# Kernel optimization log

Measured on AMD Instinct MI355X. Metric: run time of the kernel, lower is better.

## Reference

```python
import jax, jax.numpy as jnp
import numpy as np

H = 12  # num_heads

def setup_inputs() -> dict:
    key = jax.random.key(0)
    ks = jax.random.split(key, 6)
    B, L, D = 2, 2048, 768
    x = jax.random.normal(ks[0], (B, L, D), dtype=jnp.float32)
    token_sizes = jax.random.uniform(ks[1], (B, L), dtype=jnp.float32)
    attn_mask = jnp.triu(jnp.ones((L, L), dtype=bool), k=1)
    key_padding_mask = jnp.zeros((B, L), dtype=bool)
    qkv_w = jax.random.normal(ks[2], (3 * D, D), dtype=jnp.float32) * (D ** -0.5)
    qkv_b = jax.random.normal(ks[3], (3 * D,), dtype=jnp.float32) * 0.02
    proj_w = jax.random.normal(ks[4], (D, D), dtype=jnp.float32) * (D ** -0.5)
    proj_b = jax.random.normal(ks[5], (D,), dtype=jnp.float32) * 0.02
    return {"x": x, "token_sizes": token_sizes, "attn_mask": attn_mask,
            "key_padding_mask": key_padding_mask, "qkv_w": qkv_w, "qkv_b": qkv_b,
            "proj_w": proj_w, "proj_b": proj_b}

def reference(x, token_sizes, attn_mask, key_padding_mask, qkv_w, qkv_b, proj_w, proj_b):
    B, L, D = x.shape
    hd = D // H
    scale = hd ** -0.5
    qkv = (x @ qkv_w.T + qkv_b).reshape(B, L, 3, H, hd)
    qkv = jnp.transpose(qkv, (2, 0, 3, 1, 4))  # [3, B, H, L, hd]
    q, k, v = qkv[0], qkv[1], qkv[2]
    logits = jnp.einsum('bhqd,bhkd->bhqk', q, k) * scale  # [B,H,L,L]
    neg = jnp.finfo(logits.dtype).min
    logits = jnp.where(attn_mask[None, None, :, :], neg, logits)
    logits = jnp.where(key_padding_mask[:, None, None, :], neg, logits)
    logits = logits + jnp.log(jnp.clip(token_sizes, 1e-8))[:, None, None, :]
    attn = jax.nn.softmax(logits, axis=-1)
    out = jnp.einsum('bhqk,bhkd->bhqd', attn, v)
    out = jnp.transpose(out, (0, 2, 1, 3)).reshape(B, L, D)
    out = out @ proj_w.T + proj_b
    k_merge = k.mean(axis=1)  # [B, L, hd]
    return (out, k_merge)
```

## Files before the change

kernel.cpp:

```cpp
#include <hip/hip_runtime.h>
#include <hip/hip_bf16.h>

typedef unsigned short u16;
typedef __bf16 bf16x8 __attribute__((ext_vector_type(8)));
typedef float f32x4 __attribute__((ext_vector_type(4)));

#define QSCALE (0.125f * 1.44269504088896340736f)

__device__ __forceinline__ u16 f2bf(float f) {
    __hip_bfloat16 h = __float2bfloat16(f);
    return __builtin_bit_cast(u16, h);
}
__device__ __forceinline__ float bf2f(u16 u) {
    unsigned int x = ((unsigned int)u) << 16;
    return __builtin_bit_cast(float, x);
}
__device__ __forceinline__ bf16x8 ld_bf8(const u16* p) {
    uint4 u = *reinterpret_cast<const uint4*>(p);
    return __builtin_bit_cast(bf16x8, u);
}
__device__ __forceinline__ bf16x8 pack8f(f32x4 a, f32x4 b) {
    union { bf16x8 v; u16 u[8]; } r;
    #pragma unroll
    for (int i = 0; i < 4; i++) { r.u[i] = f2bf(a[i]); r.u[4+i] = f2bf(b[i]); }
    return r.v;
}
__device__ __forceinline__ bf16x8 pack8u(ushort4 a, ushort4 b) {
    union { bf16x8 v; ushort4 u[2]; } r;
    r.u[0] = a; r.u[1] = b;
    return r.v;
}

#define GLOAD_LDS16(g, l) __builtin_amdgcn_global_load_lds( \
    (const __attribute__((address_space(1))) unsigned int*)(g), \
    (__attribute__((address_space(3))) unsigned int*)(l), 16, 0, 0)

template<int N> __device__ __forceinline__ void s_wait_vmcnt() {
    if constexpr (N == 0)      asm volatile("s_waitcnt vmcnt(0)" ::: "memory");
    else if constexpr (N == 3) asm volatile("s_waitcnt vmcnt(3)" ::: "memory");
    else if constexpr (N == 4) asm volatile("s_waitcnt vmcnt(4)" ::: "memory");
    else                       asm volatile("s_waitcnt vmcnt(8)" ::: "memory");
}
__device__ __forceinline__ void s_bar() {
    __builtin_amdgcn_sched_barrier(0);
    __builtin_amdgcn_s_barrier();
    __builtin_amdgcn_sched_barrier(0);
}
__device__ __forceinline__ void s_wait_lgkm0_bar() {
    asm volatile("s_waitcnt lgkmcnt(0)" ::: "memory");
    __builtin_amdgcn_sched_barrier(0);
    __builtin_amdgcn_s_barrier();
    __builtin_amdgcn_sched_barrier(0);
}

__global__ __launch_bounds__(256) void prep_kernel(
    const float* __restrict__ x, const float* __restrict__ qkvw,
    const float* __restrict__ projw, const float* __restrict__ ts,
    const unsigned char* __restrict__ kpm,
    u16* __restrict__ Xb, u16* __restrict__ Wq, u16* __restrict__ Wp,
    float* __restrict__ tsw, u16* __restrict__ tbf, int* __restrict__ qcount)
{
    int i = blockIdx.x * 256 + threadIdx.x;
    if (i == 0) *qcount = 0;
    const int XC4 = 4096 * 768 / 4;
    const int WQ4 = 2304 * 768 / 4;
    const int WP4 = 768 * 768 / 4;
    const float* src = nullptr; u16* dst = nullptr;
    if (i < XC4) { src = x; dst = Xb; }
    else {
        i -= XC4;
        if (i < WQ4) { src = qkvw; dst = Wq; }
        else {
            i -= WQ4;
            if (i < WP4) { src = projw; dst = Wp; }
            else {
                i -= WP4;
                if (i < 1024) {
                    float4 t = *(const float4*)(ts + i*4);
                    uchar4 k = *(const uchar4*)(kpm + i*4);
                    float4 r;
                    r.x = k.x ? 0.f : fmaxf(t.x, 1e-8f);
                    r.y = k.y ? 0.f : fmaxf(t.y, 1e-8f);
                    r.z = k.z ? 0.f : fmaxf(t.z, 1e-8f);
                    r.w = k.w ? 0.f : fmaxf(t.w, 1e-8f);
                    *(float4*)(tsw + i*4) = r;
                    ushort4 o;
                    o.x = f2bf(r.x); o.y = f2bf(r.y);
                    o.z = f2bf(r.z); o.w = f2bf(r.w);
                    *(ushort4*)(tbf + i*4) = o;
                }
                return;
            }
        }
    }
    float4 v = *(const float4*)(src + i*4);
    ushort4 o;
    o.x = f2bf(v.x); o.y = f2bf(v.y); o.z = f2bf(v.z); o.w = f2bf(v.w);
    *(ushort4*)(dst + i*4) = o;
}

template<int EPI, int MI>
__global__ __launch_bounds__(256, 2) void gemm_bt(
    const u16* __restrict__ A, const u16* __restrict__ Bm,
    const float* __restrict__ bias, const float* __restrict__ tsw,
    u16* __restrict__ Qb, u16* __restrict__ Kb, u16* __restrict__ Vt,
    float* __restrict__ outp)
{
    constexpr int BM = MI * 32;
    constexpr int ACALLS = MI / 2;
    constexpr int SA = ACALLS + 2;
    constexpr int NT = 24;
    __shared__ u16 As[2][BM * 32];
    __shared__ u16 Bs[2][128 * 32];
    const int K = 768;
    const int tid = threadIdx.x;
    const int nwg = gridDim.x * gridDim.y;
    const int flat = blockIdx.y * gridDim.x + blockIdx.x;
    const int per = nwg >> 3;
    const int swz = (flat & 7) * per + (flat >> 3);
    const int m0 = (swz / gridDim.x) * BM;
    const int n0 = (swz % gridDim.x) * 128;
    const int w = tid >> 6, lane = tid & 63;
    const int wr = (w >> 1) * (MI * 16), wc = (w & 1) * 64;
    const int g = lane >> 4, l16 = lane & 15;

    const int srow = lane >> 2;
    const int scol = (lane & 3) * 8;
    const u16* gA[ACALLS];
    #pragma unroll
    for (int c = 0; c < ACALLS; c++)
        gA[c] = A + (size_t)(m0 + (c*4 + w)*16 + srow) * K + scol;
    const u16* gB[2];
    #pragma unroll
    for (int c = 0; c < 2; c++)
        gB[c] = Bm + (size_t)(n0 + (c*4 + w)*16 + srow) * K + scol;

#define GSTAGE(buf, kk) do { \
    _Pragma("unroll") \
    for (int c = 0; c < ACALLS; c++) \
        GLOAD_LDS16(gA[c] + (kk), &As[buf][(c*4 + w) * 512]); \
    _Pragma("unroll") \
    for (int c = 0; c < 2; c++) \
        GLOAD_LDS16(gB[c] + (kk), &Bs[buf][(c*4 + w) * 512]); } while (0)

    f32x4 acc[MI][4] = {};
    GSTAGE(0, 0);
    GSTAGE(1, 32);
    for (int it = 0; it < NT; it++) {
        const int k0 = it * 32;
        const int cur = it & 1;
        if (it < NT - 1) s_wait_vmcnt<SA>();
        else             s_wait_vmcnt<0>();
        s_bar();
        bf16x8 af[MI], bfr[4];
        #pragma unroll
        for (int i = 0; i < MI; i++) af[i]  = ld_bf8(&As[cur][(wr + i*16 + l16)*32 + g*8]);
        #pragma unroll
        for (int j = 0; j < 4; j++)  bfr[j] = ld_bf8(&Bs[cur][(wc + j*16 + l16)*32 + g*8]);
        s_wait_lgkm0_bar();
        if (it + 2 < NT) GSTAGE(cur, k0 + 64);
        __builtin_amdgcn_s_setprio(1);
        #pragma unroll
        for (int i = 0; i < MI; i++)
            #pragma unroll
            for (int j = 0; j < 4; j++)
                acc[i][j] = __builtin_amdgcn_mfma_f32_16x16x32_bf16(af[i], bfr[j], acc[i][j], 0, 0, 0);
        __builtin_amdgcn_s_setprio(0);
    }
#undef GSTAGE

    #pragma unroll
    for (int j = 0; j < 4; j++) {
        const int n = n0 + wc + j*16 + l16;
        const float bs = bias[n];
        #pragma unroll
        for (int i = 0; i < MI; i++) {
            #pragma unroll
            for (int r = 0; r < 4; r++) {
                const int m = m0 + wr + i*16 + g*4 + r;
                float v = acc[i][j][r] + bs;
                if (EPI == 0) {
                    int b = m >> 11, l = m & 2047;
                    unsigned int which = (unsigned int)n / 768u;
                    int rem = n - (int)which * 768;
                    int h = rem >> 6, d = rem & 63;
                    int bh = b * 12 + h;
                    if (which == 0)      Qb[((size_t)bh*2048 + l)*64 + d] = f2bf(v * QSCALE);
                    else if (which == 1) Kb[((size_t)bh*2048 + l)*64 + d] = f2bf(v);
                    else                 Vt[((size_t)bh*64 + d)*2048 + l] = f2bf(v * tsw[b*2048 + l]);
                } else {
                    outp[(size_t)m * 768 + n] = v;
                }
            }
        }
    }
}

__global__ __launch_bounds__(256, 2) void attn_kernel(
    const u16* __restrict__ Q, const u16* __restrict__ Kb,
    const u16* __restrict__ Vt, const u16* __restrict__ tbf,
    u16* __restrict__ O, int* __restrict__ qcount)
{
    __shared__ u16 Ks[2][64 * 64];
    __shared__ u16 Vs[2][64 * 64];
    __shared__ int s_item;
    const int tid = threadIdx.x;
    const int w = tid >> 6, lane = tid & 63;
    const int g = lane >> 4, l16 = lane & 15;
    const int sw = l16 & 7;
    const int srow = lane >> 3;
    const int sslot = (lane & 7) ^ srow;

    for (;;) {
        if (tid == 0) s_item = atomicAdd(qcount, 1);
        __syncthreads();
        const int item = s_item;
        if (item >= 768) return;
        const int qt = 31 - (item / 24);
        const int bh = item - (item / 24) * 24;
        const int b = bh / 12, h = bh - b * 12;
        const int q0 = qt * 64 + w * 16;
        const int nkt = qt + 1;

        const u16* Qp = Q + ((size_t)bh * 2048 + q0) * 64;
        const u16* Kp = Kb + (size_t)bh * 2048 * 64;
        const u16* Vp = Vt + (size_t)bh * 64 * 2048;
        const u16* tb = tbf + b * 2048;

        const u16* gK0 = Kp + (size_t)(w*16 +     srow) * 64   + sslot * 8;
        const u16* gK1 = Kp + (size_t)(w*16 + 8 + srow) * 64   + sslot * 8;
        const u16* gV0 = Vp + (size_t)(w*16 +     srow) * 2048 + sslot * 8;
        const u16* gV1 = Vp + (size_t)(w*16 + 8 + srow) * 2048 + sslot * 8;

#define ASTAGE(buf, kk) do { \
    GLOAD_LDS16(gK0 + (size_t)(kk) * 64, &Ks[buf][(w*16    ) * 64]); \
    GLOAD_LDS16(gK1 + (size_t)(kk) * 64, &Ks[buf][(w*16 + 8) * 64]); \
    GLOAD_LDS16(gV0 + (kk),              &Vs[buf][(w*16    ) * 64]); \
    GLOAD_LDS16(gV1 + (kk),              &Vs[buf][(w*16 + 8) * 64]); } while (0)

        const bf16x8 qf0 = ld_bf8(Qp + l16 * 64 + g * 8);
        const bf16x8 qf1 = ld_bf8(Qp + l16 * 64 + 32 + g * 8);

        ushort4 tc0, tc1, tc2, tc3;
        { const u16* tp = tb + 4*g;
          tc0 = *(const ushort4*)(tp);      tc1 = *(const ushort4*)(tp + 16);
          tc2 = *(const ushort4*)(tp + 32); tc3 = *(const ushort4*)(tp + 48); }
        ASTAGE(0, 0);

        f32x4 o[4] = {};
        f32x4 lpacc = {};
        float m = -1e30f;
        const int qmy = q0 + l16;

        for (int kt = 0; kt < nkt; kt++) {
            const int cur = kt & 1;
            const int k0 = kt * 64;

            ushort4 tn0 = tc0, tn1 = tc1, tn2 = tc2, tn3 = tc3;
            if (kt + 1 < nkt) {
                const u16* tp = tb + k0 + 64 + 4*g;
                tn0 = *(const ushort4*)(tp);      tn1 = *(const ushort4*)(tp + 16);
                tn2 = *(const ushort4*)(tp + 32); tn3 = *(const ushort4*)(tp + 48);
                ASTAGE(cur ^ 1, k0 + 64);
                s_wait_vmcnt<8>();
            } else {
                s_wait_vmcnt<0>();
            }
            s_bar();

            const int ko0 = 8 * (g ^ sw);
            bf16x8 kf[4][2];
            #pragma unroll
            for (int t = 0; t < 4; t++) {
                const u16* kb = &Ks[cur][(t*16 + l16) * 64];
                kf[t][0] = ld_bf8(kb + ko0);
                kf[t][1] = ld_bf8(kb + (ko0 ^ 32));
            }
            const int gh = g >> 1, gl = 4 * (g & 1);
            ushort4 va[4][4];
            #pragma unroll
            for (int j = 0; j < 4; j++) {
                const u16* vb = &Vs[cur][(j*16 + l16) * 64];
                va[j][0] = *(const ushort4*)(vb + (((0 + gh) ^ sw) << 3) + gl);
                va[j][1] = *(const ushort4*)(vb + (((2 + gh) ^ sw) << 3) + gl);
                va[j][2] = *(const ushort4*)(vb + (((4 + gh) ^ sw) << 3) + gl);
                va[j][3] = *(const ushort4*)(vb + (((6 + gh) ^ sw) << 3) + gl);
            }

            f32x4 s[4];
            #pragma unroll
            for (int t = 0; t < 4; t++) {
                f32x4 z = {};
                z = __builtin_amdgcn_mfma_f32_16x16x32_bf16(kf[t][0], qf0, z, 0, 0, 0);
                z = __builtin_amdgcn_mfma_f32_16x16x32_bf16(kf[t][1], qf1, z, 0, 0, 0);
                s[t] = z;
            }
            if (kt == qt) {
                #pragma unroll
                for (int t = 0; t < 4; t++)
                    #pragma unroll
                    for (int r = 0; r < 4; r++) {
                        const int key = k0 + t*16 + 4*g + r;
                        if (key > qmy) s[t][r] = -1e30f;
                    }
            }
            float pmax = -1e30f;
            #pragma unroll
            for (int t = 0; t < 4; t++)
                #pragma unroll
                for (int r = 0; r < 4; r++)
                    pmax = fmaxf(pmax, s[t][r]);
            pmax = fmaxf(pmax, __shfl_xor(pmax, 16));
            pmax = fmaxf(pmax, __shfl_xor(pmax, 32));
            if (!__all(pmax <= m + 8.f)) {
                const float mn = fmaxf(m, pmax);
                const float sc = __builtin_amdgcn_exp2f(m - mn);
                m = mn;
                #pragma unroll
                for (int r = 0; r < 4; r++) {
                    const float scr = __shfl(sc, (lane & 48) + 4*g + r);
                    o[0][r] *= scr; o[1][r] *= scr; o[2][r] *= scr; o[3][r] *= scr;
                    lpacc[r] *= scr;
                }
            }
            #pragma unroll
            for (int t = 0; t < 4; t++)
                #pragma unroll
                for (int r = 0; r < 4; r++)
                    s[t][r] = __builtin_amdgcn_exp2f(s[t][r] - m);
            const bf16x8 pa01 = pack8f(s[0], s[1]);
            const bf16x8 pa23 = pack8f(s[2], s[3]);
            __builtin_amdgcn_s_setprio(1);
            lpacc = __builtin_amdgcn_mfma_f32_16x16x32_bf16(pa01, pack8u(tc0, tc1), lpacc, 0, 0, 0);
            lpacc = __builtin_amdgcn_mfma_f32_16x16x32_bf16(pa23, pack8u(tc2, tc3), lpacc, 0, 0, 0);
            #pragma unroll
            for (int j = 0; j < 4; j++) {
                o[j] = __builtin_amdgcn_mfma_f32_16x16x32_bf16(pa01, pack8u(va[j][0], va[j][1]), o[j], 0, 0, 0);
                o[j] = __builtin_amdgcn_mfma_f32_16x16x32_bf16(pa23, pack8u(va[j][2], va[j][3]), o[j], 0, 0, 0);
            }
            __builtin_amdgcn_s_setprio(0);
            s_wait_lgkm0_bar();
            tc0 = tn0; tc1 = tn1; tc2 = tn2; tc3 = tn3;
        }
#undef ASTAGE

        float rlr[4];
        #pragma unroll
        for (int r = 0; r < 4; r++) rlr[r] = 1.f / lpacc[r];
        #pragma unroll
        for (int j = 0; j < 4; j++)
            #pragma unroll
            for (int r = 0; r < 4; r++) {
                const int q = q0 + 4*g + r;
                O[((size_t)b*2048 + q)*768 + h*64 + j*16 + l16] = f2bf(o[j][r] * rlr[r]);
            }
    }
}

__global__ __launch_bounds__(256) void kmerge_kernel(
    const u16* __restrict__ Kb, float* __restrict__ out)
{
    const int idx = blockIdx.x * 256 + threadIdx.x;
    const int d4 = (idx & 15) * 4;
    const int l = (idx >> 4) & 2047;
    const int b = idx >> 15;
    float4 acc = {0.f, 0.f, 0.f, 0.f};
    #pragma unroll
    for (int h = 0; h < 12; h++) {
        ushort4 v = *(const ushort4*)&Kb[(((size_t)(b*12 + h))*2048 + l)*64 + d4];
        acc.x += bf2f(v.x); acc.y += bf2f(v.y);
        acc.z += bf2f(v.z); acc.w += bf2f(v.w);
    }
    const float s = 1.f / 12.f;
    float4 r = {acc.x * s, acc.y * s, acc.z * s, acc.w * s};
    *(float4*)&out[(((size_t)b*2048 + l))*64 + d4] = r;
}

extern "C" void kernel_launch(void* const* d_in, const int* in_sizes, int n_in,
                              void* d_out, int out_size, void* d_ws, size_t ws_size,
                              hipStream_t stream)
{
    const float* x     = (const float*)d_in[0];
    const float* ts    = (const float*)d_in[1];
    const unsigned char* kpm = (const unsigned char*)d_in[3];
    const float* qkvw  = (const float*)d_in[4];
    const float* qkvb  = (const float*)d_in[5];
    const float* projw = (const float*)d_in[6];
    const float* projb = (const float*)d_in[7];
    float* out = (float*)d_out;

    char* ws = (char*)d_ws;
    u16* Xb = (u16*)ws;  ws += (size_t)4096 * 768 * 2;
    u16* Wq = (u16*)ws;  ws += (size_t)2304 * 768 * 2;
    u16* Wp = (u16*)ws;  ws += (size_t)768 * 768 * 2;
    u16* Qb = (u16*)ws;  ws += (size_t)24 * 2048 * 64 * 2;
    u16* Kb = (u16*)ws;  ws += (size_t)24 * 2048 * 64 * 2;
    u16* Vt = (u16*)ws;  ws += (size_t)24 * 2048 * 64 * 2;
    u16* Ob = (u16*)ws;  ws += (size_t)4096 * 768 * 2;
    float* tsw = (float*)ws;  ws += (size_t)2 * 2048 * 4;
    u16* tbf = (u16*)ws;  ws += (size_t)2 * 2048 * 2;
    int* qcount = (int*)ws;

    const int prep4 = (4096*768 + 2304*768 + 768*768) / 4 + 1024;
    prep_kernel<<<(prep4 + 255) / 256, 256, 0, stream>>>(
        x, qkvw, projw, ts, kpm, Xb, Wq, Wp, tsw, tbf, qcount);

    gemm_bt<0, 4><<<dim3(18, 32), 256, 0, stream>>>(Xb, Wq, qkvb, tsw, Qb, Kb, Vt, nullptr);

    attn_kernel<<<dim3(512), 256, 0, stream>>>(Qb, Kb, Vt, tbf, Ob, qcount);

    kmerge_kernel<<<(2*2048*16) / 256, 256, 0, stream>>>(Kb, out + 3145728);

    gemm_bt<1, 2><<<dim3(6, 64), 256, 0, stream>>>(Ob, Wp, projb, nullptr, nullptr, nullptr, nullptr, out);
}
```

Measured before the change: 111.0 us.

## Use 128-row attention tiles, 4-stage K/V pipeline, and XCD-local work queues

The attention kernel now runs 512-thread blocks of 8 waves, each block covering 128 query rows, and stages K/V tiles through a 4-deep LDS ring with a prefetch distance of two. The trailing LDS barrier is dropped, and the QK MFMAs move ahead of the V fragment loads. Work items come from per-XCD atomic queues with a global fallback and per-item claim flags, so each XCD tends to handle its own heads and keep K/V in its local L2. The costs are more LDS per block, more complex synchronisation, and the risk of a race on the ring buffer now that the end-of-iteration barrier is gone.

```diff
diff --git a/kernel.cpp b/kernel.cpp
--- a/kernel.cpp
+++ b/kernel.cpp
@@ -36,10 +36,11 @@
     (__attribute__((address_space(3))) unsigned int*)(l), 16, 0, 0)
 
 template<int N> __device__ __forceinline__ void s_wait_vmcnt() {
-    if constexpr (N == 0)      asm volatile("s_waitcnt vmcnt(0)" ::: "memory");
-    else if constexpr (N == 3) asm volatile("s_waitcnt vmcnt(3)" ::: "memory");
-    else if constexpr (N == 4) asm volatile("s_waitcnt vmcnt(4)" ::: "memory");
-    else                       asm volatile("s_waitcnt vmcnt(8)" ::: "memory");
+    if constexpr (N == 0)       asm volatile("s_waitcnt vmcnt(0)" ::: "memory");
+    else if constexpr (N == 3)  asm volatile("s_waitcnt vmcnt(3)" ::: "memory");
+    else if constexpr (N == 4)  asm volatile("s_waitcnt vmcnt(4)" ::: "memory");
+    else if constexpr (N == 8)  asm volatile("s_waitcnt vmcnt(8)" ::: "memory");
+    else if constexpr (N == 12) asm volatile("s_waitcnt vmcnt(12)" ::: "memory");
 }
 __device__ __forceinline__ void s_bar() {
     __builtin_amdgcn_sched_barrier(0);
@@ -52,16 +53,16 @@
     __builtin_amdgcn_s_barrier();
     __builtin_amdgcn_sched_barrier(0);
 }
+__device__ __forceinline__ void sched_fence() { __builtin_amdgcn_sched_barrier(0); }
 
 __global__ __launch_bounds__(256) void prep_kernel(
     const float* __restrict__ x, const float* __restrict__ qkvw,
     const float* __restrict__ projw, const float* __restrict__ ts,
     const unsigned char* __restrict__ kpm,
     u16* __restrict__ Xb, u16* __restrict__ Wq, u16* __restrict__ Wp,
-    float* __restrict__ tsw, u16* __restrict__ tbf, int* __restrict__ qcount)
+    float* __restrict__ tsw, u16* __restrict__ tbf, int* __restrict__ qarr)
 {
     int i = blockIdx.x * 256 + threadIdx.x;
-    if (i == 0) *qcount = 0;
     const int XC4 = 4096 * 768 / 4;
     const int WQ4 = 2304 * 768 / 4;
     const int WP4 = 768 * 768 / 4;
@@ -88,7 +89,10 @@
                     o.x = f2bf(r.x); o.y = f2bf(r.y);
                     o.z = f2bf(r.z); o.w = f2bf(r.w);
                     *(ushort4*)(tbf + i*4) = o;
+                    return;
                 }
+                i -= 1024;
+                if (i < 512) qarr[i] = 0;
                 return;
             }
         }
@@ -196,13 +200,13 @@
     }
 }
 
-__global__ __launch_bounds__(256, 2) void attn_kernel(
+__global__ __launch_bounds__(512, 4) void attn_kernel(
     const u16* __restrict__ Q, const u16* __restrict__ Kb,
     const u16* __restrict__ Vt, const u16* __restrict__ tbf,
-    u16* __restrict__ O, int* __restrict__ qcount)
+    u16* __restrict__ O, int* __restrict__ qarr)
 {
-    __shared__ u16 Ks[2][64 * 64];
-    __shared__ u16 Vs[2][64 * 64];
+    __shared__ u16 Ks[4][64 * 64];
+    __shared__ u16 Vs[4][64 * 64];
     __shared__ int s_item;
     const int tid = threadIdx.x;
     const int w = tid >> 6, lane = tid & 63;
@@ -210,42 +214,59 @@
     const int sw = l16 & 7;
     const int srow = lane >> 3;
     const int sslot = (lane & 7) ^ srow;
+    int xcd;
+    asm("s_getreg_b32 %0, hwreg(HW_REG_XCC_ID)" : "=s"(xcd));
+    xcd &= 7;
+    int* qc = qarr;
+    int* fl = qarr + 9;
 
     for (;;) {
-        if (tid == 0) s_item = atomicAdd(qcount, 1);
+        if (tid == 0) {
+            int it = -1;
+            for (;;) {
+                int i = atomicAdd(&qc[xcd], 1);
+                int id;
+                if (i < 48) {
+                    id = (15 - i/3) * 24 + xcd*3 + (i - (i/3)*3);
+                } else {
+                    int g2 = atomicAdd(&qc[8], 1);
+                    if (g2 >= 384) break;
+                    id = (15 - g2/24) * 24 + (g2 - (g2/24)*24);
+                }
+                if (atomicExch(&fl[id], 1) == 0) { it = id; break; }
+            }
+            s_item = it;
+        }
         __syncthreads();
         const int item = s_item;
-        if (item >= 768) return;
-        const int qt = 31 - (item / 24);
-        const int bh = item - (item / 24) * 24;
+        if (item < 0) return;
+        const int qt2 = item / 24, bh = item - qt2*24;
         const int b = bh / 12, h = bh - b * 12;
-        const int q0 = qt * 64 + w * 16;
-        const int nkt = qt + 1;
+        const int q0 = qt2 * 128 + w * 16;
+        const int nkt = 2*qt2 + 2;
 
         const u16* Qp = Q + ((size_t)bh * 2048 + q0) * 64;
         const u16* Kp = Kb + (size_t)bh * 2048 * 64;
         const u16* Vp = Vt + (size_t)bh * 64 * 2048;
         const u16* tb = tbf + b * 2048;
 
-        const u16* gK0 = Kp + (size_t)(w*16 +     srow) * 64   + sslot * 8;
-        const u16* gK1 = Kp + (size_t)(w*16 + 8 + srow) * 64   + sslot * 8;
-        const u16* gV0 = Vp + (size_t)(w*16 +     srow) * 2048 + sslot * 8;
-        const u16* gV1 = Vp + (size_t)(w*16 + 8 + srow) * 2048 + sslot * 8;
+        const u16* gK = Kp + (size_t)(w*8 + srow) * 64   + sslot * 8;
+        const u16* gV = Vp + (size_t)(w*8 + srow) * 2048 + sslot * 8;
 
 #define ASTAGE(buf, kk) do { \
-    GLOAD_LDS16(gK0 + (size_t)(kk) * 64, &Ks[buf][(w*16    ) * 64]); \
-    GLOAD_LDS16(gK1 + (size_t)(kk) * 64, &Ks[buf][(w*16 + 8) * 64]); \
-    GLOAD_LDS16(gV0 + (kk),              &Vs[buf][(w*16    ) * 64]); \
-    GLOAD_LDS16(gV1 + (kk),              &Vs[buf][(w*16 + 8) * 64]); } while (0)
+    GLOAD_LDS16(gK + (size_t)(kk) * 64, &Ks[buf][(w*8) * 64]); \
+    GLOAD_LDS16(gV + (kk),              &Vs[buf][(w*8) * 64]); } while (0)
 
         const bf16x8 qf0 = ld_bf8(Qp + l16 * 64 + g * 8);
         const bf16x8 qf1 = ld_bf8(Qp + l16 * 64 + 32 + g * 8);
-
         ushort4 tc0, tc1, tc2, tc3;
         { const u16* tp = tb + 4*g;
           tc0 = *(const ushort4*)(tp);      tc1 = *(const ushort4*)(tp + 16);
           tc2 = *(const ushort4*)(tp + 32); tc3 = *(const ushort4*)(tp + 48); }
+        sched_fence();
         ASTAGE(0, 0);
+        ASTAGE(1, 64);
+        sched_fence();
 
         f32x4 o[4] = {};
         f32x4 lpacc = {};
@@ -253,7 +274,7 @@
         const int qmy = q0 + l16;
 
         for (int kt = 0; kt < nkt; kt++) {
-            const int cur = kt & 1;
+            const int cur = kt & 3;
             const int k0 = kt * 64;
 
             ushort4 tn0 = tc0, tn1 = tc1, tn2 = tc2, tn3 = tc3;
@@ -261,11 +282,13 @@
                 const u16* tp = tb + k0 + 64 + 4*g;
                 tn0 = *(const ushort4*)(tp);      tn1 = *(const ushort4*)(tp + 16);
                 tn2 = *(const ushort4*)(tp + 32); tn3 = *(const ushort4*)(tp + 48);
-                ASTAGE(cur ^ 1, k0 + 64);
-                s_wait_vmcnt<8>();
-            } else {
-                s_wait_vmcnt<0>();
-            }
+            }
+            sched_fence();
+            if (kt + 2 < nkt) ASTAGE((kt + 2) & 3, k0 + 128);
+            sched_fence();
+            if (kt >= 1 && kt + 2 < nkt)      s_wait_vmcnt<12>();
+            else if (kt == 0 && nkt > 2)      s_wait_vmcnt<8>();
+            else                              s_wait_vmcnt<0>();
             s_bar();
 
             const int ko0 = 8 * (g ^ sw);
@@ -275,6 +298,14 @@
                 const u16* kb = &Ks[cur][(t*16 + l16) * 64];
                 kf[t][0] = ld_bf8(kb + ko0);
                 kf[t][1] = ld_bf8(kb + (ko0 ^ 32));
+            }
+            f32x4 s[4];
+            #pragma unroll
+            for (int t = 0; t < 4; t++) {
+                f32x4 z = {};
+                z = __builtin_amdgcn_mfma_f32_16x16x32_bf16(kf[t][0], qf0, z, 0, 0, 0);
+                z = __builtin_amdgcn_mfma_f32_16x16x32_bf16(kf[t][1], qf1, z, 0, 0, 0);
+                s[t] = z;
             }
             const int gh = g >> 1, gl = 4 * (g & 1);
             ushort4 va[4][4];
@@ -286,16 +317,7 @@
                 va[j][2] = *(const ushort4*)(vb + (((4 + gh) ^ sw) << 3) + gl);
                 va[j][3] = *(const ushort4*)(vb + (((6 + gh) ^ sw) << 3) + gl);
             }
-
-            f32x4 s[4];
-            #pragma unroll
-            for (int t = 0; t < 4; t++) {
-                f32x4 z = {};
-                z = __builtin_amdgcn_mfma_f32_16x16x32_bf16(kf[t][0], qf0, z, 0, 0, 0);
-                z = __builtin_amdgcn_mfma_f32_16x16x32_bf16(kf[t][1], qf1, z, 0, 0, 0);
-                s[t] = z;
-            }
-            if (kt == qt) {
+            if (kt >= nkt - 2) {
                 #pragma unroll
                 for (int t = 0; t < 4; t++)
                     #pragma unroll
@@ -339,7 +361,6 @@
                 o[j] = __builtin_amdgcn_mfma_f32_16x16x32_bf16(pa23, pack8u(va[j][2], va[j][3]), o[j], 0, 0, 0);
             }
             __builtin_amdgcn_s_setprio(0);
-            s_wait_lgkm0_bar();
             tc0 = tn0; tc1 = tn1; tc2 = tn2; tc3 = tn3;
         }
 #undef ASTAGE
@@ -399,15 +420,15 @@
     u16* Ob = (u16*)ws;  ws += (size_t)4096 * 768 * 2;
     float* tsw = (float*)ws;  ws += (size_t)2 * 2048 * 4;
     u16* tbf = (u16*)ws;  ws += (size_t)2 * 2048 * 2;
-    int* qcount = (int*)ws;
-
-    const int prep4 = (4096*768 + 2304*768 + 768*768) / 4 + 1024;
+    int* qarr = (int*)ws;
+
+    const int prep4 = (4096*768 + 2304*768 + 768*768) / 4 + 1024 + 512;
     prep_kernel<<<(prep4 + 255) / 256, 256, 0, stream>>>(
-        x, qkvw, projw, ts, kpm, Xb, Wq, Wp, tsw, tbf, qcount);
+        x, qkvw, projw, ts, kpm, Xb, Wq, Wp, tsw, tbf, qarr);
 
     gemm_bt<0, 4><<<dim3(18, 32), 256, 0, stream>>>(Xb, Wq, qkvb, tsw, Qb, Kb, Vt, nullptr);
 
-    attn_kernel<<<dim3(512), 256, 0, stream>>>(Qb, Kb, Vt, tbf, Ob, qcount);
+    attn_kernel<<<dim3(512), 512, 0, stream>>>(Qb, Kb, Vt, tbf, Ob, qarr);
 
     kmerge_kernel<<<(2*2048*16) / 256, 256, 0, stream>>>(Kb, out + 3145728);
 
```

Result: slower. 118.4 us (+6.7%).

## Schedule attention work per XCD for L2 locality and simplify load waits

Applied to the files above, without the earlier changes.

Replaces the single global atomic work counter in the attention kernel with per-XCD counters. Each XCD first claims items from its own fixed subset of heads, then falls back to a global counter, with atomicExch claim flags preventing duplicate work. The aim is to keep each head's K/V tiles resident in one XCD's L2. The explicit vmcnt waits and LDS barriers in the attention K-loop become plain __syncthreads, which may lose some prefetch overlap. The setprio hints around the GEMM MFMA loop are also removed.

```diff
diff --git a/kernel.cpp b/kernel.cpp
--- a/kernel.cpp
+++ b/kernel.cpp
@@ -36,10 +36,9 @@
     (__attribute__((address_space(3))) unsigned int*)(l), 16, 0, 0)
 
 template<int N> __device__ __forceinline__ void s_wait_vmcnt() {
-    if constexpr (N == 0)      asm volatile("s_waitcnt vmcnt(0)" ::: "memory");
-    else if constexpr (N == 3) asm volatile("s_waitcnt vmcnt(3)" ::: "memory");
-    else if constexpr (N == 4) asm volatile("s_waitcnt vmcnt(4)" ::: "memory");
-    else                       asm volatile("s_waitcnt vmcnt(8)" ::: "memory");
+    if constexpr (N == 0)       asm volatile("s_waitcnt vmcnt(0)" ::: "memory");
+    else if constexpr (N == 3)  asm volatile("s_waitcnt vmcnt(3)" ::: "memory");
+    else if constexpr (N == 4)  asm volatile("s_waitcnt vmcnt(4)" ::: "memory");
 }
 __device__ __forceinline__ void s_bar() {
     __builtin_amdgcn_sched_barrier(0);
@@ -58,10 +57,9 @@
     const float* __restrict__ projw, const float* __restrict__ ts,
     const unsigned char* __restrict__ kpm,
     u16* __restrict__ Xb, u16* __restrict__ Wq, u16* __restrict__ Wp,
-    float* __restrict__ tsw, u16* __restrict__ tbf, int* __restrict__ qcount)
+    float* __restrict__ tsw, u16* __restrict__ tbf, int* __restrict__ qarr)
 {
     int i = blockIdx.x * 256 + threadIdx.x;
-    if (i == 0) *qcount = 0;
     const int XC4 = 4096 * 768 / 4;
     const int WQ4 = 2304 * 768 / 4;
     const int WP4 = 768 * 768 / 4;
@@ -88,7 +86,10 @@
                     o.x = f2bf(r.x); o.y = f2bf(r.y);
                     o.z = f2bf(r.z); o.w = f2bf(r.w);
                     *(ushort4*)(tbf + i*4) = o;
+                    return;
                 }
+                i -= 1024;
+                if (i < 1024) qarr[i] = 0;
                 return;
             }
         }
@@ -159,13 +160,11 @@
         for (int j = 0; j < 4; j++)  bfr[j] = ld_bf8(&Bs[cur][(wc + j*16 + l16)*32 + g*8]);
         s_wait_lgkm0_bar();
         if (it + 2 < NT) GSTAGE(cur, k0 + 64);
-        __builtin_amdgcn_s_setprio(1);
         #pragma unroll
         for (int i = 0; i < MI; i++)
             #pragma unroll
             for (int j = 0; j < 4; j++)
                 acc[i][j] = __builtin_amdgcn_mfma_f32_16x16x32_bf16(af[i], bfr[j], acc[i][j], 0, 0, 0);
-        __builtin_amdgcn_s_setprio(0);
     }
 #undef GSTAGE
 
@@ -199,7 +198,7 @@
 __global__ __launch_bounds__(256, 2) void attn_kernel(
     const u16* __restrict__ Q, const u16* __restrict__ Kb,
     const u16* __restrict__ Vt, const u16* __restrict__ tbf,
-    u16* __restrict__ O, int* __restrict__ qcount)
+    u16* __restrict__ O, int* __restrict__ qarr)
 {
     __shared__ u16 Ks[2][64 * 64];
     __shared__ u16 Vs[2][64 * 64];
@@ -210,14 +209,36 @@
     const int sw = l16 & 7;
     const int srow = lane >> 3;
     const int sslot = (lane & 7) ^ srow;
+    int xcd;
+    asm("s_getreg_b32 %0, hwreg(HW_REG_XCC_ID)" : "=s"(xcd));
+    xcd &= 7;
+    int* qc = qarr;
+    int* fl = qarr + 9;
 
     for (;;) {
-        if (tid == 0) s_item = atomicAdd(qcount, 1);
+        if (tid == 0) {
+            int it = -1;
+            for (;;) {
+                int i = atomicAdd(&qc[xcd], 1);
+                int id;
+                if (i < 96) {
+                    int qi = i / 3;
+                    id = (31 - qi) * 24 + xcd*3 + (i - qi*3);
+                } else {
+                    int g2 = atomicAdd(&qc[8], 1);
+                    if (g2 >= 768) break;
+                    int qi = g2 / 24;
+                    id = (31 - qi) * 24 + (g2 - qi*24);
+                }
+                if (atomicExch(&fl[id], 1) == 0) { it = id; break; }
+            }
+            s_item = it;
+        }
         __syncthreads();
         const int item = s_item;
-        if (item >= 768) return;
-        const int qt = 31 - (item / 24);
-        const int bh = item - (item / 24) * 24;
+        if (item < 0) return;
+        const int qt = item / 24;
+        const int bh = item - qt * 24;
         const int b = bh / 12, h = bh - b * 12;
         const int q0 = qt * 64 + w * 16;
         const int nkt = qt + 1;
@@ -251,6 +272,8 @@
         f32x4 lpacc = {};
         float m = -1e30f;
         const int qmy = q0 + l16;
+
+        __syncthreads();
 
         for (int kt = 0; kt < nkt; kt++) {
             const int cur = kt & 1;
@@ -262,11 +285,7 @@
                 tn0 = *(const ushort4*)(tp);      tn1 = *(const ushort4*)(tp + 16);
                 tn2 = *(const ushort4*)(tp + 32); tn3 = *(const ushort4*)(tp + 48);
                 ASTAGE(cur ^ 1, k0 + 64);
-                s_wait_vmcnt<8>();
-            } else {
-                s_wait_vmcnt<0>();
-            }
-            s_bar();
+            }
 
             const int ko0 = 8 * (g ^ sw);
             bf16x8 kf[4][2];
@@ -339,7 +358,7 @@
                 o[j] = __builtin_amdgcn_mfma_f32_16x16x32_bf16(pa23, pack8u(va[j][2], va[j][3]), o[j], 0, 0, 0);
             }
             __builtin_amdgcn_s_setprio(0);
-            s_wait_lgkm0_bar();
+            __syncthreads();
             tc0 = tn0; tc1 = tn1; tc2 = tn2; tc3 = tn3;
         }
 #undef ASTAGE
@@ -399,15 +418,15 @@
     u16* Ob = (u16*)ws;  ws += (size_t)4096 * 768 * 2;
     float* tsw = (float*)ws;  ws += (size_t)2 * 2048 * 4;
     u16* tbf = (u16*)ws;  ws += (size_t)2 * 2048 * 2;
-    int* qcount = (int*)ws;
-
-    const int prep4 = (4096*768 + 2304*768 + 768*768) / 4 + 1024;
+    int* qarr = (int*)ws;
+
+    const int prep4 = (4096*768 + 2304*768 + 768*768) / 4 + 1024 + 1024;
     prep_kernel<<<(prep4 + 255) / 256, 256, 0, stream>>>(
-        x, qkvw, projw, ts, kpm, Xb, Wq, Wp, tsw, tbf, qcount);
+        x, qkvw, projw, ts, kpm, Xb, Wq, Wp, tsw, tbf, qarr);
 
     gemm_bt<0, 4><<<dim3(18, 32), 256, 0, stream>>>(Xb, Wq, qkvb, tsw, Qb, Kb, Vt, nullptr);
 
-    attn_kernel<<<dim3(512), 256, 0, stream>>>(Qb, Kb, Vt, tbf, Ob, qcount);
+    attn_kernel<<<dim3(512), 256, 0, stream>>>(Qb, Kb, Vt, tbf, Ob, qarr);
 
     kmerge_kernel<<<(2*2048*16) / 256, 256, 0, stream>>>(Kb, out + 3145728);
 
```

After: 131.2 us. +18.2%, slower.
